# Kernel optimization log

Hardware: AMD Instinct MI355X
Metric: run time of the kernel (lower is better)

Reference implementation:

```python
import jax, jax.numpy as jnp
import numpy as np

STRIDE = 8
OUT = 96                 # feature map size fh = fw
SEARCH = OUT * STRIDE    # 768, search image size
RATIOS = [0.33, 0.5, 1.0, 2.0, 3.0]
SCALES = [4, 8, 16]
PRE_NMS = 1024
POST_NMS = 256
NMS_THRESH = 0.7


def _make_anchors():
    # anchor widths/heights per (ratio, scale), base size = stride * scale
    ws, hs = [], []
    for r in RATIOS:
        for s in SCALES:
            ws.append(STRIDE * s / np.sqrt(r))
            hs.append(STRIDE * s * np.sqrt(r))
    ws = np.asarray(ws, np.float32)  # [A]
    hs = np.asarray(hs, np.float32)
    ori = SEARCH // 2 - (OUT // 2) * STRIDE
    c = ori + STRIDE * np.arange(OUT, dtype=np.float32)
    cy, cx = np.meshgrid(c, c, indexing="ij")  # [OUT, OUT]
    x1 = cx[None] - ws[:, None, None] * 0.5  # [A, OUT, OUT]
    y1 = cy[None] - hs[:, None, None] * 0.5
    x2 = cx[None] + ws[:, None, None] * 0.5
    y2 = cy[None] + hs[:, None, None] * 0.5
    return np.stack([x1, y1, x2, y2], axis=-1).reshape(-1, 4)  # [A*K, 4]


def setup_inputs() -> dict:
    key = jax.random.key(0)
    k1, k2 = jax.random.split(key)
    pred_cls = jax.random.normal(k1, (32, 30, 96, 96), jnp.float32)
    pred_reg = jax.random.normal(k2, (32, 60, 96, 96), jnp.float32) * 0.2
    anchors = jnp.asarray(_make_anchors())
    return {"pred_cls": pred_cls, "pred_reg": pred_reg, "anchors": anchors}


def _nms_pad(boxes, scores):
    """boxes [N,4] sorted by score desc, scores [N]. Returns [POST_NMS,5] padded."""
    x1, y1, x2, y2 = boxes[:, 0], boxes[:, 1], boxes[:, 2], boxes[:, 3]
    areas = (x2 - x1 + 1.0) * (y2 - y1 + 1.0)
    ix1 = jnp.maximum(x1[:, None], x1[None, :])
    iy1 = jnp.maximum(y1[:, None], y1[None, :])
    ix2 = jnp.minimum(x2[:, None], x2[None, :])
    iy2 = jnp.minimum(y2[:, None], y2[None, :])
    inter = jnp.maximum(ix2 - ix1 + 1.0, 0.0) * jnp.maximum(iy2 - iy1 + 1.0, 0.0)
    iou = inter / (areas[:, None] + areas[None, :] - inter)
    n = boxes.shape[0]
    idxs = jnp.arange(n)

    def body(keep, i):
        sup = keep[i] & (iou[i] > NMS_THRESH) & (idxs > i)
        return keep & ~sup, None

    keep, _ = jax.lax.scan(body, jnp.ones((n,), bool), idxs)
    pos = jnp.cumsum(keep) - 1
    dst = jnp.where(keep & (pos < POST_NMS), pos, POST_NMS)  # pad row for dropped
    rows = jnp.concatenate([scores[:, None], boxes], axis=1)  # [N,5] score first
    out = jnp.zeros((POST_NMS + 1, 5), boxes.dtype).at[dst].set(rows)
    return out[:POST_NMS]


def reference(pred_cls, pred_reg, anchors):
    b, a2, h, w = pred_cls.shape
    A = a2 // 2
    # log-softmax over the 2-way fg/bg channel; take foreground log-probs
    logp = jax.nn.log_softmax(pred_cls.reshape(b, 2, A, h, w), axis=1)
    scores = logp[:, 1].reshape(b, -1)  # [b, A*h*w]
    # deltas: (b,4A,h,w) -> (b,4,A,h,w) -> (b,A,h,w,4) -> (b,A*h*w,4)
    deltas = pred_reg.reshape(b, 4, A, h, w).transpose(0, 2, 3, 4, 1).reshape(b, -1, 4)
    aw = anchors[:, 2] - anchors[:, 0] + 1.0
    ah = anchors[:, 3] - anchors[:, 1] + 1.0
    acx = anchors[:, 0] + 0.5 * aw
    acy = anchors[:, 1] + 0.5 * ah
    dx, dy, dw, dh = deltas[..., 0], deltas[..., 1], deltas[..., 2], deltas[..., 3]
    pcx = dx * aw + acx
    pcy = dy * ah + acy
    pw = jnp.exp(dw) * aw
    ph = jnp.exp(dh) * ah
    boxes = jnp.stack([pcx - 0.5 * pw, pcy - 0.5 * ph, pcx + 0.5 * pw, pcy + 0.5 * ph], axis=-1)
    boxes = jnp.clip(boxes, 0.0, SEARCH - 1.0)  # clip to image
    top_s, top_i = jax.lax.top_k(scores, PRE_NMS)  # per-image pre-NMS top-k
    top_b = jnp.take_along_axis(boxes, top_i[..., None], axis=1)  # [b,PRE,4]
    return jax.vmap(_nms_pad)(top_b, top_s)  # [b, POST_NMS, 5]
```

## Files before the change

kernel.cpp:

```cpp
#include <hip/hip_runtime.h>
#include <stdint.h>

#define NANCH 138240
#define NANCH4 34560
#define B_CNT 32
#define PRE 1024
#define POST 256
#define BINS 8192
#define CAP 4096
#define SBLK 15
#define SLICE4 2304
#define TLOC 192
#define LOCCAP 273
#define SORTN 512
#define PAD_KEY 0xFFFFFFFFFFFFFFFFull

typedef unsigned long long u64;

__device__ __forceinline__ unsigned key32(float sc) {
    unsigned u = __float_as_uint(sc);
    unsigned s = (u & 0x80000000u) ? ~u : (u | 0x80000000u);
    return ~s;
}

__device__ __forceinline__ unsigned key_of(float x0, float x1) {
    float m  = fmaxf(x0, x1);
    float e0 = expf(x0 - m);
    float e1 = expf(x1 - m);
    float sc = (x1 - m) - logf(e0 + e1);
    return key32(sc);
}

__device__ __forceinline__ void decode_box(const float* __restrict__ reg,
                                           const float* __restrict__ anch,
                                           int b, int idx, float box[4]) {
    const float* rb = reg + (size_t)b * 4 * NANCH;
    float dx = rb[idx];
    float dy = rb[idx + NANCH];
    float dw = rb[idx + 2 * NANCH];
    float dh = rb[idx + 3 * NANCH];
    float ax1 = anch[idx * 4 + 0], ay1 = anch[idx * 4 + 1];
    float ax2 = anch[idx * 4 + 2], ay2 = anch[idx * 4 + 3];
    float aw  = __fadd_rn(__fsub_rn(ax2, ax1), 1.0f);
    float ah  = __fadd_rn(__fsub_rn(ay2, ay1), 1.0f);
    float acx = __fadd_rn(ax1, __fmul_rn(0.5f, aw));
    float acy = __fadd_rn(ay1, __fmul_rn(0.5f, ah));
    float pcx = __fadd_rn(__fmul_rn(dx, aw), acx);
    float pcy = __fadd_rn(__fmul_rn(dy, ah), acy);
    float pw  = __fmul_rn(expf(dw), aw);
    float ph  = __fmul_rn(expf(dh), ah);
    float hx  = __fmul_rn(0.5f, pw);
    float hy  = __fmul_rn(0.5f, ph);
    box[0] = fminf(fmaxf(__fsub_rn(pcx, hx), 0.0f), 767.0f);
    box[1] = fminf(fmaxf(__fsub_rn(pcy, hy), 0.0f), 767.0f);
    box[2] = fminf(fmaxf(__fadd_rn(pcx, hx), 0.0f), 767.0f);
    box[3] = fminf(fmaxf(__fadd_rn(pcy, hy), 0.0f), 767.0f);
}

__global__ __launch_bounds__(1024) void select_kernel(const float* __restrict__ cls,
                                                      u64* __restrict__ cand) {
    __shared__ unsigned h[BINS];
    __shared__ u64 sortbuf[SORTN];
    __shared__ unsigned s_wsum[16];
    __shared__ int s_b;
    __shared__ int lcnt;
    const int b = blockIdx.y;
    const int s = blockIdx.x;
    const int t = threadIdx.x;
    const int lane = t & 63, wid = t >> 6;
    if (t == 0) lcnt = 0;
    for (int i = t; i < BINS; i += 1024) h[i] = 0;
    if (t < SORTN) sortbuf[t] = PAD_KEY;
    __syncthreads();

    const float4* cb4 = (const float4*)(cls + (size_t)b * 2 * NANCH);
    const int base4 = s * SLICE4;

    unsigned kk[3][4];
    #pragma unroll
    for (int k = 0; k < 3; ++k) {
        int off = k * 1024 + t;
        if (off < SLICE4) {
            int g4 = base4 + off;
            float4 a0 = cb4[g4];
            float4 a1 = cb4[g4 + NANCH4];
            kk[k][0] = key_of(a0.x, a1.x);
            kk[k][1] = key_of(a0.y, a1.y);
            kk[k][2] = key_of(a0.z, a1.z);
            kk[k][3] = key_of(a0.w, a1.w);
            atomicAdd(&h[kk[k][0] >> 19], 1u);
            atomicAdd(&h[kk[k][1] >> 19], 1u);
            atomicAdd(&h[kk[k][2] >> 19], 1u);
            atomicAdd(&h[kk[k][3] >> 19], 1u);
        }
    }
    __syncthreads();

    unsigned bin[8];
    unsigned seg = 0;
    #pragma unroll
    for (int i = 0; i < 8; ++i) { bin[i] = h[t * 8 + i]; seg += bin[i]; }
    unsigned sc = seg;
    #pragma unroll
    for (int o = 1; o < 64; o <<= 1) {
        unsigned v = (unsigned)__shfl_up((int)sc, o);
        if (lane >= o) sc += v;
    }
    if (lane == 63) s_wsum[wid] = sc;
    __syncthreads();
    unsigned woff = 0;
    for (int i = 0; i < wid; ++i) woff += s_wsum[i];
    unsigned incl = sc + woff;
    unsigned excl = incl - seg;
    if (incl >= TLOC && excl < TLOC) {
        unsigned cum = excl;
        int bs = t * 8 + 7;
        for (int i = 0; i < 8; ++i) {
            if (cum + bin[i] >= TLOC) { bs = t * 8 + i; break; }
            cum += bin[i];
        }
        s_b = bs;
    }
    __syncthreads();
    const int bs = s_b;

    #pragma unroll
    for (int k = 0; k < 3; ++k) {
        int off = k * 1024 + t;
        if (off < SLICE4) {
            int g4 = base4 + off;
            #pragma unroll
            for (int j = 0; j < 4; ++j) {
                unsigned key = kk[k][j];
                if ((int)(key >> 19) <= bs) {
                    int pos = atomicAdd(&lcnt, 1);
                    if (pos < LOCCAP)
                        sortbuf[pos] = ((u64)key << 32) | (unsigned)(g4 * 4 + j);
                }
            }
        }
    }
    __syncthreads();

    for (int k = 2; k <= SORTN; k <<= 1) {
        for (int j = k >> 1; j > 0; j >>= 1) {
            if (t < SORTN / 2) {
                int i = ((t & ~(j - 1)) << 1) | (t & (j - 1));
                int p = i | j;
                bool up = ((i & k) == 0);
                u64 a = sortbuf[i], bb = sortbuf[p];
                if ((a > bb) == up) { sortbuf[i] = bb; sortbuf[p] = a; }
            }
            __syncthreads();
        }
    }

    u64* segp = cand + (size_t)b * CAP + s * LOCCAP;
    for (int i = t; i < LOCCAP; i += 1024) segp[i] = sortbuf[i];
    if (s == 0 && t == 0) cand[(size_t)b * CAP + (CAP - 1)] = PAD_KEY;
}

__global__ __launch_bounds__(512) void merge_kernel(const u64* __restrict__ cand,
                                                    const float* __restrict__ reg,
                                                    const float* __restrict__ anch,
                                                    float* __restrict__ topS,
                                                    float* __restrict__ topB) {
    __shared__ u64 runs[CAP];
    const int b = blockIdx.y;
    const int t = threadIdx.x;
    const int slot = blockIdx.x * 512 + t;
    for (int i = t; i < CAP; i += 512) runs[i] = cand[(size_t)b * CAP + i];
    __syncthreads();

    u64 x = runs[slot];
    if (x == PAD_KEY) return;
    const int r = slot / LOCCAP;
    int rank = slot - r * LOCCAP;
    for (int q = 0; q < SBLK; ++q) {
        if (q == r) continue;
        const u64* run = &runs[q * LOCCAP];
        int lo = 0, hi = LOCCAP;
        while (lo < hi) {
            int mid = (lo + hi) >> 1;
            if (run[mid] < x) lo = mid + 1; else hi = mid;
        }
        rank += lo;
    }
    if (rank < PRE) {
        int idx = (int)(x & 0xFFFFFFFFu);
        unsigned ks = (unsigned)(x >> 32);
        unsigned s  = ~ks;
        unsigned u  = (s & 0x80000000u) ? (s & 0x7FFFFFFFu) : ~s;
        float scv = __uint_as_float(u);
        float box[4];
        decode_box(reg, anch, b, idx, box);
        topS[b * PRE + rank] = scv;
        float* tb = topB + ((size_t)b * PRE + rank) * 4;
        tb[0] = box[0]; tb[1] = box[1]; tb[2] = box[2]; tb[3] = box[3];
    }
}

__global__ __launch_bounds__(1024) void mask_kernel(const float* __restrict__ topB,
                                                    u64* __restrict__ masks) {
    const int w = blockIdx.x;
    const int b = blockIdx.y;
    const int i = threadIdx.x;
    __shared__ float sx1[64], sy1[64], sx2[64], sy2[64], sar[64];
    if (i < 64) {
        const float* p = topB + ((size_t)b * PRE + w * 64 + i) * 4;
        float x1 = p[0], y1 = p[1], x2 = p[2], y2 = p[3];
        sx1[i] = x1; sy1[i] = y1; sx2[i] = x2; sy2[i] = y2;
        sar[i] = __fmul_rn(__fadd_rn(__fsub_rn(x2, x1), 1.0f),
                           __fadd_rn(__fsub_rn(y2, y1), 1.0f));
    }
    __syncthreads();
    const int jbase = w * 64;
    u64* dst = &masks[((size_t)b * PRE + i) * 16 + w];
    if (i >= jbase + 63) { *dst = 0ull; return; }
    const float* p = topB + ((size_t)b * PRE + i) * 4;
    float x1 = p[0], y1 = p[1], x2 = p[2], y2 = p[3];
    float ar = __fmul_rn(__fadd_rn(__fsub_rn(x2, x1), 1.0f),
                         __fadd_rn(__fsub_rn(y2, y1), 1.0f));
    u64 m = 0ull;
    for (int j = 0; j < 64; j++) {
        int jj = jbase + j;
        if (jj > i) {
            float ix1 = fmaxf(x1, sx1[j]);
            float iy1 = fmaxf(y1, sy1[j]);
            float ix2 = fminf(x2, sx2[j]);
            float iy2 = fminf(y2, sy2[j]);
            float iw = fmaxf(__fadd_rn(__fsub_rn(ix2, ix1), 1.0f), 0.0f);
            float ih = fmaxf(__fadd_rn(__fsub_rn(iy2, iy1), 1.0f), 0.0f);
            float inter = __fmul_rn(iw, ih);
            float denom = __fsub_rn(__fadd_rn(ar, sar[j]), inter);
            float iou = __fdiv_rn(inter, denom);
            if (iou > 0.7f) m |= (1ull << j);
        }
    }
    *dst = m;
}

__device__ __forceinline__ u64 shfl_xor_u64(u64 v, int lanemask) {
    int lo = __shfl_xor((int)(v & 0xFFFFFFFFull), lanemask);
    int hi = __shfl_xor((int)(v >> 32), lanemask);
    return ((u64)(unsigned)hi << 32) | (unsigned)lo;
}

__global__ __launch_bounds__(64) void nms_kernel(const u64* __restrict__ masks,
                                                 const float* __restrict__ topS,
                                                 const float* __restrict__ topB,
                                                 float* __restrict__ out) {
    const int b = blockIdx.x;
    const int t = threadIdx.x;
    __shared__ u64 rem[16];
    __shared__ int kept[POST];
    __shared__ int s_nk;
    if (t < 16) rem[t] = 0ull;
    __syncthreads();

    const u64* mb = masks + (size_t)b * PRE * 16;
    const int w = t >> 2, g = t & 3;
    int prefix = 0;

    u64 dv_cur = mb[(size_t)t * 16 + 0];
    u64 cw_cur[16];
    #pragma unroll
    for (int k = 0; k < 16; ++k)
        cw_cur[k] = mb[((size_t)(g * 16 + k)) * 16 + w];

    for (int c = 0; c < 16; ++c) {
        u64 dv_nxt = 0ull;
        u64 cw_nxt[16];
        if (c < 15) {
            const u64* nb = mb + (size_t)(c + 1) * 64 * 16;
            dv_nxt = nb[(size_t)t * 16 + (c + 1)];
            #pragma unroll
            for (int k = 0; k < 16; ++k)
                cw_nxt[k] = nb[((size_t)(g * 16 + k)) * 16 + w];
        } else {
            #pragma unroll
            for (int k = 0; k < 16; ++k) cw_nxt[k] = 0ull;
        }

        u64 alive = ~rem[c];
        int dlo = (int)(dv_cur & 0xFFFFFFFFull);
        int dhi = (int)(dv_cur >> 32);

        for (int l = 0; l < 64; ++l) {
            unsigned lo = (unsigned)__builtin_amdgcn_readlane(dlo, l);
            unsigned hi = (unsigned)__builtin_amdgcn_readlane(dhi, l);
            u64 dl = ((u64)hi << 32) | lo;
            u64 a = (alive >> l) & 1ull;
            alive &= ~(a ? dl : 0ull);
        }

        if ((alive >> t) & 1ull) {
            int pos = prefix + (int)__popcll(alive & ((1ull << t) - 1ull));
            if (pos < POST) kept[pos] = c * 64 + t;
        }
        prefix += (int)__popcll(alive);

        u64 acc = 0ull;
        #pragma unroll
        for (int k = 0; k < 16; ++k)
            if ((alive >> (g * 16 + k)) & 1ull) acc |= cw_cur[k];
        acc |= shfl_xor_u64(acc, 1);
        acc |= shfl_xor_u64(acc, 2);
        __syncthreads();
        if (g == 0 && w > c) rem[w] |= acc;
        __syncthreads();

        if (prefix >= POST) break;

        dv_cur = dv_nxt;
        #pragma unroll
        for (int k = 0; k < 16; ++k) cw_cur[k] = cw_nxt[k];
    }

    if (t == 0) s_nk = (prefix < POST) ? prefix : POST;
    __syncthreads();
    const int n = s_nk;

    float* ob = out + (size_t)b * POST * 5;
    for (int r = t; r < POST; r += 64) {
        if (r < n) {
            int i = kept[r];
            ob[r * 5 + 0] = topS[b * PRE + i];
            const float* tb = topB + ((size_t)b * PRE + i) * 4;
            ob[r * 5 + 1] = tb[0];
            ob[r * 5 + 2] = tb[1];
            ob[r * 5 + 3] = tb[2];
            ob[r * 5 + 4] = tb[3];
        } else {
            ob[r * 5 + 0] = 0.0f; ob[r * 5 + 1] = 0.0f; ob[r * 5 + 2] = 0.0f;
            ob[r * 5 + 3] = 0.0f; ob[r * 5 + 4] = 0.0f;
        }
    }
}

extern "C" void kernel_launch(void* const* d_in, const int* in_sizes, int n_in,
                              void* d_out, int out_size, void* d_ws, size_t ws_size,
                              hipStream_t stream) {
    const float* cls  = (const float*)d_in[0];
    const float* reg  = (const float*)d_in[1];
    const float* anch = (const float*)d_in[2];

    char* ws = (char*)d_ws;
    float* topS  = (float*)ws;
    float* topB  = (float*)(ws + 131072);
    u64*   cand  = (u64*)(ws + 655360);
    u64*   masks = (u64*)(ws + 1703936);

    select_kernel<<<dim3(SBLK, B_CNT), 1024, 0, stream>>>(cls, cand);
    merge_kernel <<<dim3(8, B_CNT), 512, 0, stream>>>(cand, reg, anch, topS, topB);
    mask_kernel  <<<dim3(16, B_CNT), 1024, 0, stream>>>(topB, masks);
    nms_kernel   <<<B_CNT, 64, 0, stream>>>(masks, topS, topB, (float*)d_out);
}
```

Measured before the change: 83.86 us.

## Fuse IoU mask computation into NMS kernel using shared-memory masks

```diff
diff --git a/kernel.cpp b/kernel.cpp
--- a/kernel.cpp
+++ b/kernel.cpp
@@ -13,6 +13,7 @@
 #define TLOC 192
 #define LOCCAP 273
 #define SORTN 512
+#define SMROW 17
 #define PAD_KEY 0xFFFFFFFFFFFFFFFFull
 
 typedef unsigned long long u64;
@@ -29,6 +30,19 @@
     float e1 = expf(x1 - m);
     float sc = (x1 - m) - logf(e0 + e1);
     return key32(sc);
+}
+
+__device__ __forceinline__ bool iou_gt(float x1, float y1, float x2, float y2, float ar,
+                                       float ox1, float oy1, float ox2, float oy2, float oar) {
+    float ix1 = fmaxf(x1, ox1);
+    float iy1 = fmaxf(y1, oy1);
+    float ix2 = fminf(x2, ox2);
+    float iy2 = fminf(y2, oy2);
+    float iw = fmaxf(__fadd_rn(__fsub_rn(ix2, ix1), 1.0f), 0.0f);
+    float ih = fmaxf(__fadd_rn(__fsub_rn(iy2, iy1), 1.0f), 0.0f);
+    float inter = __fmul_rn(iw, ih);
+    float denom = __fsub_rn(__fadd_rn(ar, oar), inter);
+    return __fdiv_rn(inter, denom) > 0.7f;
 }
 
 __device__ __forceinline__ void decode_box(const float* __restrict__ reg,
@@ -57,6 +71,17 @@
     box[3] = fminf(fmaxf(__fadd_rn(pcy, hy), 0.0f), 767.0f);
 }
 
+__device__ __forceinline__ u64 shfl_xor_u64(u64 v, int lanemask) {
+    int lo = __shfl_xor((int)(v & 0xFFFFFFFFull), lanemask);
+    int hi = __shfl_xor((int)(v >> 32), lanemask);
+    return ((u64)(unsigned)hi << 32) | (unsigned)lo;
+}
+__device__ __forceinline__ u64 shfl_u64(u64 v, int srcLane) {
+    int lo = __shfl((int)(v & 0xFFFFFFFFull), srcLane);
+    int hi = __shfl((int)(v >> 32), srcLane);
+    return ((u64)(unsigned)hi << 32) | (unsigned)lo;
+}
+
 __global__ __launch_bounds__(1024) void select_kernel(const float* __restrict__ cls,
                                                       u64* __restrict__ cand) {
     __shared__ unsigned h[BINS];
@@ -200,140 +225,93 @@
     }
 }
 
-__global__ __launch_bounds__(1024) void mask_kernel(const float* __restrict__ topB,
-                                                    u64* __restrict__ masks) {
-    const int w = blockIdx.x;
-    const int b = blockIdx.y;
-    const int i = threadIdx.x;
-    __shared__ float sx1[64], sy1[64], sx2[64], sy2[64], sar[64];
-    if (i < 64) {
-        const float* p = topB + ((size_t)b * PRE + w * 64 + i) * 4;
-        float x1 = p[0], y1 = p[1], x2 = p[2], y2 = p[3];
-        sx1[i] = x1; sy1[i] = y1; sx2[i] = x2; sy2[i] = y2;
-        sar[i] = __fmul_rn(__fadd_rn(__fsub_rn(x2, x1), 1.0f),
-                           __fadd_rn(__fsub_rn(y2, y1), 1.0f));
-    }
-    __syncthreads();
-    const int jbase = w * 64;
-    u64* dst = &masks[((size_t)b * PRE + i) * 16 + w];
-    if (i >= jbase + 63) { *dst = 0ull; return; }
-    const float* p = topB + ((size_t)b * PRE + i) * 4;
-    float x1 = p[0], y1 = p[1], x2 = p[2], y2 = p[3];
-    float ar = __fmul_rn(__fadd_rn(__fsub_rn(x2, x1), 1.0f),
-                         __fadd_rn(__fsub_rn(y2, y1), 1.0f));
-    u64 m = 0ull;
-    for (int j = 0; j < 64; j++) {
-        int jj = jbase + j;
-        if (jj > i) {
-            float ix1 = fmaxf(x1, sx1[j]);
-            float iy1 = fmaxf(y1, sy1[j]);
-            float ix2 = fminf(x2, sx2[j]);
-            float iy2 = fminf(y2, sy2[j]);
-            float iw = fmaxf(__fadd_rn(__fsub_rn(ix2, ix1), 1.0f), 0.0f);
-            float ih = fmaxf(__fadd_rn(__fsub_rn(iy2, iy1), 1.0f), 0.0f);
-            float inter = __fmul_rn(iw, ih);
-            float denom = __fsub_rn(__fadd_rn(ar, sar[j]), inter);
-            float iou = __fdiv_rn(inter, denom);
-            if (iou > 0.7f) m |= (1ull << j);
-        }
-    }
-    *dst = m;
-}
-
-__device__ __forceinline__ u64 shfl_xor_u64(u64 v, int lanemask) {
-    int lo = __shfl_xor((int)(v & 0xFFFFFFFFull), lanemask);
-    int hi = __shfl_xor((int)(v >> 32), lanemask);
-    return ((u64)(unsigned)hi << 32) | (unsigned)lo;
-}
-
-__global__ __launch_bounds__(64) void nms_kernel(const u64* __restrict__ masks,
-                                                 const float* __restrict__ topS,
-                                                 const float* __restrict__ topB,
-                                                 float* __restrict__ out) {
+__global__ __launch_bounds__(1024) void nms_kernel(const float* __restrict__ topS,
+                                                   const float* __restrict__ topB,
+                                                   float* __restrict__ out) {
+    __shared__ u64 smask[PRE * SMROW];
+    __shared__ float sx1[PRE], sy1[PRE], sx2[PRE], sy2[PRE], sar[PRE];
+    __shared__ int kept[POST];
+    __shared__ int s_nk;
     const int b = blockIdx.x;
     const int t = threadIdx.x;
-    __shared__ u64 rem[16];
-    __shared__ int kept[POST];
-    __shared__ int s_nk;
-    if (t < 16) rem[t] = 0ull;
-    __syncthreads();
-
-    const u64* mb = masks + (size_t)b * PRE * 16;
-    const int w = t >> 2, g = t & 3;
-    int prefix = 0;
-
-    u64 dv_cur = mb[(size_t)t * 16 + 0];
-    u64 cw_cur[16];
-    #pragma unroll
-    for (int k = 0; k < 16; ++k)
-        cw_cur[k] = mb[((size_t)(g * 16 + k)) * 16 + w];
-
-    for (int c = 0; c < 16; ++c) {
-        u64 dv_nxt = 0ull;
-        u64 cw_nxt[16];
-        if (c < 15) {
-            const u64* nb = mb + (size_t)(c + 1) * 64 * 16;
-            dv_nxt = nb[(size_t)t * 16 + (c + 1)];
+
+    float4 bx = ((const float4*)topB)[(size_t)b * PRE + t];
+    sx1[t] = bx.x; sy1[t] = bx.y; sx2[t] = bx.z; sy2[t] = bx.w;
+    sar[t] = __fmul_rn(__fadd_rn(__fsub_rn(bx.z, bx.x), 1.0f),
+                       __fadd_rn(__fsub_rn(bx.w, bx.y), 1.0f));
+    __syncthreads();
+
+    {
+        float x1 = sx1[t], y1 = sy1[t], x2 = sx2[t], y2 = sy2[t], ar = sar[t];
+        const int wlo = t >> 6;
+        for (int w = 0; w < 16; ++w) {
+            u64 m = 0ull;
+            if (w >= wlo) {
+                const int jbase = w * 64;
+                for (int j = 0; j < 64; ++j) {
+                    int jj = jbase + j;
+                    if (jj > t && iou_gt(x1, y1, x2, y2, ar,
+                                         sx1[jj], sy1[jj], sx2[jj], sy2[jj], sar[jj]))
+                        m |= (1ull << j);
+                }
+            }
+            smask[t * SMROW + w] = m;
+        }
+    }
+    __syncthreads();
+
+    if (t < 64) {
+        const int lane = t;
+        const int w = lane >> 2, g = lane & 3;
+        u64 remreg = 0ull;
+        int prefix = 0;
+        for (int c = 0; c < 16; ++c) {
+            u64 alive = ~shfl_u64(remreg, c);
+            u64 dv = smask[(c * 64 + lane) * SMROW + c];
+            int dlo = (int)(dv & 0xFFFFFFFFull);
+            int dhi = (int)(dv >> 32);
+            for (int l = 0; l < 64; ++l) {
+                unsigned lo = (unsigned)__builtin_amdgcn_readlane(dlo, l);
+                unsigned hi = (unsigned)__builtin_amdgcn_readlane(dhi, l);
+                u64 dl = ((u64)hi << 32) | lo;
+                u64 a = (alive >> l) & 1ull;
+                alive &= ~(a ? dl : 0ull);
+            }
+            if ((alive >> lane) & 1ull) {
+                int pos = prefix + (int)__popcll(alive & ((1ull << lane) - 1ull));
+                if (pos < POST) kept[pos] = c * 64 + lane;
+            }
+            prefix += (int)__popcll(alive);
+
+            u64 acc = 0ull;
             #pragma unroll
             for (int k = 0; k < 16; ++k)
-                cw_nxt[k] = nb[((size_t)(g * 16 + k)) * 16 + w];
+                if ((alive >> (g * 16 + k)) & 1ull)
+                    acc |= smask[(c * 64 + g * 16 + k) * SMROW + w];
+            acc |= shfl_xor_u64(acc, 1);
+            acc |= shfl_xor_u64(acc, 2);
+            u64 val = shfl_u64(acc, (lane & 15) * 4);
+            if (lane < 16 && lane > c) remreg |= val;
+
+            if (prefix >= POST) break;
+        }
+        if (lane == 0) s_nk = (prefix < POST) ? prefix : POST;
+    }
+    __syncthreads();
+
+    const int n = s_nk;
+    float* ob = out + (size_t)b * POST * 5;
+    if (t < POST) {
+        if (t < n) {
+            int i = kept[t];
+            ob[t * 5 + 0] = topS[b * PRE + i];
+            ob[t * 5 + 1] = sx1[i];
+            ob[t * 5 + 2] = sy1[i];
+            ob[t * 5 + 3] = sx2[i];
+            ob[t * 5 + 4] = sy2[i];
         } else {
-            #pragma unroll
-            for (int k = 0; k < 16; ++k) cw_nxt[k] = 0ull;
-        }
-
-        u64 alive = ~rem[c];
-        int dlo = (int)(dv_cur & 0xFFFFFFFFull);
-        int dhi = (int)(dv_cur >> 32);
-
-        for (int l = 0; l < 64; ++l) {
-            unsigned lo = (unsigned)__builtin_amdgcn_readlane(dlo, l);
-            unsigned hi = (unsigned)__builtin_amdgcn_readlane(dhi, l);
-            u64 dl = ((u64)hi << 32) | lo;
-            u64 a = (alive >> l) & 1ull;
-            alive &= ~(a ? dl : 0ull);
-        }
-
-        if ((alive >> t) & 1ull) {
-            int pos = prefix + (int)__popcll(alive & ((1ull << t) - 1ull));
-            if (pos < POST) kept[pos] = c * 64 + t;
-        }
-        prefix += (int)__popcll(alive);
-
-        u64 acc = 0ull;
-        #pragma unroll
-        for (int k = 0; k < 16; ++k)
-            if ((alive >> (g * 16 + k)) & 1ull) acc |= cw_cur[k];
-        acc |= shfl_xor_u64(acc, 1);
-        acc |= shfl_xor_u64(acc, 2);
-        __syncthreads();
-        if (g == 0 && w > c) rem[w] |= acc;
-        __syncthreads();
-
-        if (prefix >= POST) break;
-
-        dv_cur = dv_nxt;
-        #pragma unroll
-        for (int k = 0; k < 16; ++k) cw_cur[k] = cw_nxt[k];
-    }
-
-    if (t == 0) s_nk = (prefix < POST) ? prefix : POST;
-    __syncthreads();
-    const int n = s_nk;
-
-    float* ob = out + (size_t)b * POST * 5;
-    for (int r = t; r < POST; r += 64) {
-        if (r < n) {
-            int i = kept[r];
-            ob[r * 5 + 0] = topS[b * PRE + i];
-            const float* tb = topB + ((size_t)b * PRE + i) * 4;
-            ob[r * 5 + 1] = tb[0];
-            ob[r * 5 + 2] = tb[1];
-            ob[r * 5 + 3] = tb[2];
-            ob[r * 5 + 4] = tb[3];
-        } else {
-            ob[r * 5 + 0] = 0.0f; ob[r * 5 + 1] = 0.0f; ob[r * 5 + 2] = 0.0f;
-            ob[r * 5 + 3] = 0.0f; ob[r * 5 + 4] = 0.0f;
+            ob[t * 5 + 0] = 0.0f; ob[t * 5 + 1] = 0.0f; ob[t * 5 + 2] = 0.0f;
+            ob[t * 5 + 3] = 0.0f; ob[t * 5 + 4] = 0.0f;
         }
     }
 }
@@ -349,10 +327,8 @@
     float* topS  = (float*)ws;
     float* topB  = (float*)(ws + 131072);
     u64*   cand  = (u64*)(ws + 655360);
-    u64*   masks = (u64*)(ws + 1703936);
 
     select_kernel<<<dim3(SBLK, B_CNT), 1024, 0, stream>>>(cls, cand);
     merge_kernel <<<dim3(8, B_CNT), 512, 0, stream>>>(cand, reg, anch, topS, topB);
-    mask_kernel  <<<dim3(16, B_CNT), 1024, 0, stream>>>(topB, masks);
-    nms_kernel   <<<B_CNT, 64, 0, stream>>>(masks, topS, topB, (float*)d_out);
-}
+    nms_kernel   <<<B_CNT, 1024, 0, stream>>>(topS, topB, (float*)d_out);
+}
```

Measured after the change: 210.5 us. 151% more time.
